# Kernel optimization log

Hardware: AMD Instinct MI355X
Metric: run time of the kernel (lower is better)

The kernel has to match this reference:

```python
import jax, jax.numpy as jnp
import numpy as np

T = 16          # time_span
N = 128         # num_trajectory
D = 512         # embedding dim
TEMP = 0.1      # temperature
INF = 1000000000.0
M = 2 * N * T   # total rows of z (two views)


def setup_inputs() -> dict:
    key = jax.random.key(0)
    k1, k2 = jax.random.split(key)
    z = jax.random.normal(k1, (M, D), dtype=jnp.float32)
    done = jax.random.randint(k2, (T, N), 0, 2).astype(jnp.int32)  # [T, N] binary done flags
    return {"z": z, "done": done}


def _build_positive_mask(done):
    # done: [T, N] int -> transposed to [N, T] as in the torch code
    d = done.astype(jnp.float32).T  # [N, T]
    # Sequential rewrite loop is equivalent to:
    #   done_new[r,t] = 1 iff exists original done at p < t in row r AND orig done[r,t] == 0
    excl = jnp.cumsum(d, axis=1) - d  # exclusive cumsum along time
    d_new = jnp.where((excl > 0) & (d == 0), 1.0, 0.0)  # [N, T]
    done_vec = 1.0 - d_new.reshape(-1)  # [N*T]
    # block-diagonal temporal mask: same trajectory => 1
    traj = jnp.arange(N * T) // T
    block = (traj[:, None] == traj[None, :]).astype(jnp.float32)  # [NT, NT]
    done_mask = (done_vec[:, None] * done_vec[None, :]) * block
    done_mask = jnp.tile(done_mask, (2, 2))      # [M, M]
    temporal_mask = jnp.tile(block, (2, 2))      # [M, M]
    eye = jnp.eye(M, dtype=jnp.float32)
    positive_mask = (1.0 - done_mask) * (1.0 - temporal_mask) + eye
    return positive_mask, eye


def reference(z, done):
    positive_mask, eye = _build_positive_mask(done)
    # cosine similarity = normalize + GEMM (same math as broadcasted F.cosine_similarity)
    norms = jnp.maximum(jnp.linalg.norm(z, axis=-1, keepdims=True), 1e-8)
    zn = z / norms
    logits = (zn @ zn.T) / TEMP - eye * INF  # [M, M]
    log_probs = jax.nn.log_softmax(logits, axis=1)
    neg = 1.0 - positive_mask
    mean_log_prob = jnp.sum(neg * log_probs, axis=1) / jnp.sum(neg, axis=1)
    return -jnp.mean(mean_log_prob)
```

## Files before the change

kernel.cpp:

```cpp
#include <hip/hip_runtime.h>
#include <hip/hip_bf16.h>

typedef float f32x16 __attribute__((ext_vector_type(16)));
typedef unsigned short u16;
typedef unsigned char u8;
typedef unsigned int u32;
typedef unsigned long long u64;


__device__ inline void async_cp16(const u8* g, u8* l) {
    __builtin_amdgcn_global_load_lds(
        (const __attribute__((address_space(1))) unsigned int*)g,
        (__attribute__((address_space(3))) unsigned int*)l, 16, 0, 0);
}

__global__ void nrm_kernel(const float* __restrict__ z, u8* __restrict__ zn8) {
    int row = blockIdx.x;
    int tid = threadIdx.x;
    float4 v = ((const float4*)(z + row * 512))[tid];
    float ss = v.x * v.x + v.y * v.y + v.z * v.z + v.w * v.w;
#pragma unroll
    for (int off = 32; off; off >>= 1) ss += __shfl_down(ss, off, 64);
    __shared__ float red[2];
    if ((tid & 63) == 0) red[tid >> 6] = ss;
    __syncthreads();
    float sc = 1.0f / fmaxf(sqrtf(red[0] + red[1]), 1e-8f);
    u32 w = __builtin_amdgcn_cvt_pk_fp8_f32(v.x * sc, v.y * sc, 0, false);
    w = __builtin_amdgcn_cvt_pk_fp8_f32(v.z * sc, v.w * sc, w, true);
    ((u32*)(zn8 + (size_t)row * 512))[tid] = w;
}

__global__ void pos_kernel(const u8* __restrict__ zn8, float* __restrict__ possum) {
    int g = blockIdx.x;
    int l = threadIdx.x;
    int u = l & 31, h = l >> 5;
    int grow = (u < 16) ? (g * 16 + u) : (2048 + g * 16 + (u - 16));
    const u64* src = (const u64*)(zn8 + (size_t)grow * 512);
    f32x16 acc = {};
#pragma unroll
    for (int kc = 0; kc < 32; ++kc) {
        u64 f = src[2 * kc + h];
        acc = __builtin_amdgcn_mfma_f32_32x32x16_fp8_fp8((long)f, (long)f, acc, 0, 0, 0);
    }
#pragma unroll
    for (int r = 0; r < 16; ++r) {
        int rrow = (r & 3) + 8 * (r >> 2) + 4 * h;
        float v = (rrow == u) ? 0.f : acc[r];
        v += __shfl_xor(v, 1, 64);
        v += __shfl_xor(v, 2, 64);
        v += __shfl_xor(v, 4, 64);
        v += __shfl_xor(v, 8, 64);
        v += __shfl_xor(v, 16, 64);
        if (u == 0) {
            int gr = (rrow < 16) ? (g * 16 + rrow) : (2048 + g * 16 + (rrow - 16));
            possum[gr] = v * 10.0f;
        }
    }
}

__global__ __launch_bounds__(256, 3) void gemm_kernel(const u8* __restrict__ zn8,
                                                      float* __restrict__ part) {
    __shared__ u8 Bt[2][32 * 512];
    __shared__ float colred[4][4][32];
    __shared__ float rowred[128];
    int wave = threadIdx.x >> 6;
    int l = threadIdx.x & 63;
    int m = l & 31, h = l >> 5;

    int t = blockIdx.x, i = 0;
    while (t >= 32 - i) { t -= 32 - i; ++i; }
    int j = i + t;
    int rowbase = i * 128 + wave * 32;
    bool diagwg = (i == j);

    long af[32];
    {
        const u8* arow = zn8 + (size_t)(rowbase + m) * 512 + h * 8;
#pragma unroll
        for (int kc = 0; kc < 32; ++kc) af[kc] = *(const long*)(arow + kc * 16);
    }

    float expacc[16];
#pragma unroll
    for (int r = 0; r < 16; ++r) expacc[r] = 0.f;

    auto stage = [&](int buf, int ct) {
        int colbase = j * 128 + ct * 32;
#pragma unroll
        for (int it = 0; it < 4; ++it) {
            int c = wave * 8 + 2 * it;
            int C = colbase + c + h;
            int srcoff = (m ^ (C & 7)) * 16;
            async_cp16(zn8 + (size_t)C * 512 + srcoff, &Bt[buf][c * 512]);
        }
    };

    stage(0, 0);
    int sB16 = (m & 7) * 16;
    for (int ct = 0; ct < 4; ++ct) {
        __syncthreads();
        if (ct < 3) stage((ct + 1) & 1, ct + 1);
        const u8* bcol = &Bt[ct & 1][m * 512 + h * 8];
        f32x16 acc = {};
#pragma unroll
        for (int kc = 0; kc < 32; ++kc) {
            u64 bf = *(const u64*)(bcol + ((kc * 16) ^ sB16));
            acc = __builtin_amdgcn_mfma_f32_32x32x16_fp8_fp8(af[kc], (long)bf, acc, 0, 0, 0);
        }
        bool diagtile = diagwg && (ct == wave);
        float cs = 0.f;
#pragma unroll
        for (int r = 0; r < 16; ++r) {
            int rrow = (r & 3) + 8 * (r >> 2) + 4 * h;
            float e = (diagtile && rrow == m) ? 0.f : __expf(acc[r] * 10.0f);
            expacc[r] += e;
            cs += e;
        }
        cs += __shfl_xor(cs, 32, 64);
        if (h == 0) colred[wave][ct][m] = cs;
    }

#pragma unroll
    for (int r = 0; r < 16; ++r) {
        float v = expacc[r];
        v += __shfl_xor(v, 1, 64);
        v += __shfl_xor(v, 2, 64);
        v += __shfl_xor(v, 4, 64);
        v += __shfl_xor(v, 8, 64);
        v += __shfl_xor(v, 16, 64);
        if (m == 0) {
            int rrow = (r & 3) + 8 * (r >> 2) + 4 * h;
            rowred[wave * 32 + rrow] = v;
        }
    }
    __syncthreads();
    if (threadIdx.x < 128) {
        int tid = threadIdx.x;
        part[(size_t)(i * 32 + j) * 128 + tid] = rowred[tid];
        if (!diagwg) {
            int tt = tid >> 5, c2 = tid & 31;
            float cv = colred[0][tt][c2] + colred[1][tt][c2] +
                       colred[2][tt][c2] + colred[3][tt][c2];
            part[(size_t)(j * 32 + i) * 128 + tid] = cv;
        }
    }
}

__global__ void fin_kernel(const float* __restrict__ part,
                           const float* __restrict__ possum, float* __restrict__ out) {
    int tid = threadIdx.x;
    float s = 0.f;
    for (int r = tid; r < 4096; r += 1024) {
        int b = r >> 7, rr = r & 127;
        float es = 0.f;
#pragma unroll
        for (int sl = 0; sl < 32; ++sl) es += part[(size_t)(b * 32 + sl) * 128 + rr];
        s += __logf(es) - possum[r] * (1.0f / 31.0f);
    }
#pragma unroll
    for (int off = 32; off; off >>= 1) s += __shfl_down(s, off, 64);
    __shared__ float red[16];
    if ((tid & 63) == 0) red[tid >> 6] = s;
    __syncthreads();
    if (tid == 0) {
        float tt = 0.f;
#pragma unroll
        for (int i2 = 0; i2 < 16; ++i2) tt += red[i2];
        out[0] = tt * (1.0f / 4096.0f);
    }
}

extern "C" void kernel_launch(void* const* d_in, const int* in_sizes, int n_in,
                              void* d_out, int out_size, void* d_ws, size_t ws_size,
                              hipStream_t stream) {
    const float* z = (const float*)d_in[0];
    u8* zn8 = (u8*)d_ws;
    float* part = (float*)((char*)d_ws + (2u << 20));
    float* possum = part + 32 * 32 * 128;
    float* out = (float*)d_out;

    nrm_kernel<<<4096, 128, 0, stream>>>(z, zn8);
    pos_kernel<<<128, 64, 0, stream>>>(zn8, possum);
    gemm_kernel<<<528, 256, 0, stream>>>(zn8, part);
    fin_kernel<<<1, 1024, 0, stream>>>(part, possum, out);
}
```

Measured before the change: 99.40 us.

## Fuse normalize, positive-sum, GEMM and finalize into one persistent kernel with grid barriers

Replaces the four separate launches with a single persistent kernel of 512 workgroups that synchronise through atomic-counter grid barriers. Normalisation, the positive-sum MFMA pass, the tiled exp GEMM and the final log reduction now run as phases of that one kernel, and the last reduction is spread across all workgroups. The MFMA inner loop is also split into two independent accumulators to shorten the dependency chain. This removes launch gaps and the single-block finalize, at the cost of a memset, spin-wait barriers that require every workgroup to be co-resident, and 16 leftover GEMM jobs handled by a second loop iteration.

```diff
diff --git a/kernel.cpp b/kernel.cpp
--- a/kernel.cpp
+++ b/kernel.cpp
@@ -2,10 +2,11 @@
 #include <hip/hip_bf16.h>
 
 typedef float f32x16 __attribute__((ext_vector_type(16)));
-typedef unsigned short u16;
 typedef unsigned char u8;
 typedef unsigned int u32;
 typedef unsigned long long u64;
+
+#define NWG 512
 
 
 __device__ inline void async_cp16(const u8* g, u8* l) {
@@ -14,159 +15,192 @@
         (__attribute__((address_space(3))) unsigned int*)l, 16, 0, 0);
 }
 
-__global__ void nrm_kernel(const float* __restrict__ z, u8* __restrict__ zn8) {
-    int row = blockIdx.x;
-    int tid = threadIdx.x;
-    float4 v = ((const float4*)(z + row * 512))[tid];
-    float ss = v.x * v.x + v.y * v.y + v.z * v.z + v.w * v.w;
-#pragma unroll
-    for (int off = 32; off; off >>= 1) ss += __shfl_down(ss, off, 64);
-    __shared__ float red[2];
-    if ((tid & 63) == 0) red[tid >> 6] = ss;
+__device__ inline void gridbar(u32* ctr, int ph) {
+    __threadfence();
     __syncthreads();
-    float sc = 1.0f / fmaxf(sqrtf(red[0] + red[1]), 1e-8f);
-    u32 w = __builtin_amdgcn_cvt_pk_fp8_f32(v.x * sc, v.y * sc, 0, false);
-    w = __builtin_amdgcn_cvt_pk_fp8_f32(v.z * sc, v.w * sc, w, true);
-    ((u32*)(zn8 + (size_t)row * 512))[tid] = w;
-}
-
-__global__ void pos_kernel(const u8* __restrict__ zn8, float* __restrict__ possum) {
-    int g = blockIdx.x;
-    int l = threadIdx.x;
-    int u = l & 31, h = l >> 5;
-    int grow = (u < 16) ? (g * 16 + u) : (2048 + g * 16 + (u - 16));
-    const u64* src = (const u64*)(zn8 + (size_t)grow * 512);
-    f32x16 acc = {};
-#pragma unroll
-    for (int kc = 0; kc < 32; ++kc) {
-        u64 f = src[2 * kc + h];
-        acc = __builtin_amdgcn_mfma_f32_32x32x16_fp8_fp8((long)f, (long)f, acc, 0, 0, 0);
-    }
-#pragma unroll
-    for (int r = 0; r < 16; ++r) {
-        int rrow = (r & 3) + 8 * (r >> 2) + 4 * h;
-        float v = (rrow == u) ? 0.f : acc[r];
-        v += __shfl_xor(v, 1, 64);
-        v += __shfl_xor(v, 2, 64);
-        v += __shfl_xor(v, 4, 64);
-        v += __shfl_xor(v, 8, 64);
-        v += __shfl_xor(v, 16, 64);
-        if (u == 0) {
-            int gr = (rrow < 16) ? (g * 16 + rrow) : (2048 + g * 16 + (rrow - 16));
-            possum[gr] = v * 10.0f;
-        }
-    }
-}
-
-__global__ __launch_bounds__(256, 3) void gemm_kernel(const u8* __restrict__ zn8,
-                                                      float* __restrict__ part) {
+    if (threadIdx.x == 0) {
+        __hip_atomic_fetch_add(&ctr[ph], 1u, __ATOMIC_ACQ_REL, __HIP_MEMORY_SCOPE_AGENT);
+        while (__hip_atomic_load(&ctr[ph], __ATOMIC_ACQUIRE, __HIP_MEMORY_SCOPE_AGENT) < NWG)
+            __builtin_amdgcn_s_sleep(2);
+    }
+    __syncthreads();
+    __threadfence();
+}
+
+__global__ __launch_bounds__(256, 2) void mega_kernel(
+        const float* __restrict__ z, u8* __restrict__ zn8, float* __restrict__ part,
+        float* __restrict__ possum, float* __restrict__ wgsum, u32* __restrict__ ctr,
+        float* __restrict__ out) {
     __shared__ u8 Bt[2][32 * 512];
     __shared__ float colred[4][4][32];
     __shared__ float rowred[128];
-    int wave = threadIdx.x >> 6;
-    int l = threadIdx.x & 63;
-    int m = l & 31, h = l >> 5;
-
-    int t = blockIdx.x, i = 0;
-    while (t >= 32 - i) { t -= 32 - i; ++i; }
-    int j = i + t;
-    int rowbase = i * 128 + wave * 32;
-    bool diagwg = (i == j);
-
-    long af[32];
+    __shared__ float fred[8];
+    __shared__ float red2[4];
+
+    const int wg = blockIdx.x, tid = threadIdx.x;
+    const int wave = tid >> 6, l = tid & 63;
+    const int m = l & 31, h = l >> 5;
+
     {
+        int rl = tid >> 5, c = tid & 31;
+        size_t R = (size_t)wg * 8 + rl;
+        const float4* zr = (const float4*)(z + R * 512);
+        float4 v[4];
+        float ss = 0.f;
+#pragma unroll
+        for (int k = 0; k < 4; ++k) {
+            v[k] = zr[c + 32 * k];
+            ss += v[k].x * v[k].x + v[k].y * v[k].y + v[k].z * v[k].z + v[k].w * v[k].w;
+        }
+#pragma unroll
+        for (int off = 16; off; off >>= 1) ss += __shfl_xor(ss, off, 64);
+        float sc = 1.0f / fmaxf(sqrtf(ss), 1e-8f);
+        u32* zw = (u32*)(zn8 + R * 512);
+#pragma unroll
+        for (int k = 0; k < 4; ++k) {
+            u32 w = __builtin_amdgcn_cvt_pk_fp8_f32(v[k].x * sc, v[k].y * sc, 0, false);
+            w = __builtin_amdgcn_cvt_pk_fp8_f32(v[k].z * sc, v[k].w * sc, w, true);
+            zw[c + 32 * k] = w;
+        }
+    }
+    gridbar(ctr, 0);
+
+    for (int job = wg; job < 528; job += NWG) {
+        int t = job, i = 0;
+        while (t >= 32 - i) { t -= 32 - i; ++i; }
+        int j = i + t;
+        int rowbase = i * 128 + wave * 32;
+        bool diagwg = (i == j);
+
+        __syncthreads();
+
+        long af[32];
         const u8* arow = zn8 + (size_t)(rowbase + m) * 512 + h * 8;
 #pragma unroll
         for (int kc = 0; kc < 32; ++kc) af[kc] = *(const long*)(arow + kc * 16);
-    }
-
-    float expacc[16];
-#pragma unroll
-    for (int r = 0; r < 16; ++r) expacc[r] = 0.f;
-
-    auto stage = [&](int buf, int ct) {
-        int colbase = j * 128 + ct * 32;
-#pragma unroll
-        for (int it = 0; it < 4; ++it) {
-            int c = wave * 8 + 2 * it;
-            int C = colbase + c + h;
-            int srcoff = (m ^ (C & 7)) * 16;
-            async_cp16(zn8 + (size_t)C * 512 + srcoff, &Bt[buf][c * 512]);
-        }
-    };
-
-    stage(0, 0);
-    int sB16 = (m & 7) * 16;
-    for (int ct = 0; ct < 4; ++ct) {
-        __syncthreads();
-        if (ct < 3) stage((ct + 1) & 1, ct + 1);
-        const u8* bcol = &Bt[ct & 1][m * 512 + h * 8];
+
+        float expacc[16];
+#pragma unroll
+        for (int r = 0; r < 16; ++r) expacc[r] = 0.f;
+
+        {
+            int colbase = j * 128;
+#pragma unroll
+            for (int it = 0; it < 4; ++it) {
+                int c = wave * 8 + 2 * it;
+                int C = colbase + c + h;
+                async_cp16(zn8 + (size_t)C * 512 + (m ^ (C & 7)) * 16, &Bt[0][c * 512]);
+            }
+        }
+        int sB16 = (m & 7) * 16;
+        for (int ct = 0; ct < 4; ++ct) {
+            __syncthreads();
+            if (ct < 3) {
+                int colbase = j * 128 + (ct + 1) * 32;
+                u8* dstb = &Bt[(ct + 1) & 1][0];
+#pragma unroll
+                for (int it = 0; it < 4; ++it) {
+                    int c = wave * 8 + 2 * it;
+                    int C = colbase + c + h;
+                    async_cp16(zn8 + (size_t)C * 512 + (m ^ (C & 7)) * 16, dstb + c * 512);
+                }
+            }
+            const u8* bcol = &Bt[ct & 1][m * 512 + h * 8];
+            f32x16 acc0 = {}, acc1 = {};
+#pragma unroll
+            for (int kc = 0; kc < 16; ++kc) {
+                u64 b0 = *(const u64*)(bcol + (((2 * kc) * 16) ^ sB16));
+                u64 b1 = *(const u64*)(bcol + (((2 * kc + 1) * 16) ^ sB16));
+                acc0 = __builtin_amdgcn_mfma_f32_32x32x16_fp8_fp8(af[2 * kc], (long)b0, acc0, 0, 0, 0);
+                acc1 = __builtin_amdgcn_mfma_f32_32x32x16_fp8_fp8(af[2 * kc + 1], (long)b1, acc1, 0, 0, 0);
+            }
+            bool diagtile = diagwg && (ct == wave);
+            float cs = 0.f;
+#pragma unroll
+            for (int r = 0; r < 16; ++r) {
+                int rrow = (r & 3) + 8 * (r >> 2) + 4 * h;
+                float e = (diagtile && rrow == m) ? 0.f : __expf((acc0[r] + acc1[r]) * 10.0f);
+                expacc[r] += e;
+                cs += e;
+            }
+            cs += __shfl_xor(cs, 32, 64);
+            if (h == 0) colred[wave][ct][m] = cs;
+        }
+#pragma unroll
+        for (int r = 0; r < 16; ++r) {
+            float v = expacc[r];
+            v += __shfl_xor(v, 1, 64);
+            v += __shfl_xor(v, 2, 64);
+            v += __shfl_xor(v, 4, 64);
+            v += __shfl_xor(v, 8, 64);
+            v += __shfl_xor(v, 16, 64);
+            if (m == 0) rowred[wave * 32 + ((r & 3) + 8 * (r >> 2) + 4 * h)] = v;
+        }
+        __syncthreads();
+        if (tid < 128) {
+            part[(size_t)(i * 32 + j) * 128 + tid] = rowred[tid];
+            if (!diagwg) {
+                int tt = tid >> 5, c2 = tid & 31;
+                part[(size_t)(j * 32 + i) * 128 + tid] =
+                    colred[0][tt][c2] + colred[1][tt][c2] +
+                    colred[2][tt][c2] + colred[3][tt][c2];
+            }
+        }
+    }
+    if (wg >= 384 && wg < 416) {
+        int g = (wg - 384) * 4 + wave;
+        int u = m;
+        int grow = (u < 16) ? (g * 16 + u) : (2048 + g * 16 + (u - 16));
+        const u64* src = (const u64*)(zn8 + (size_t)grow * 512);
         f32x16 acc = {};
 #pragma unroll
         for (int kc = 0; kc < 32; ++kc) {
-            u64 bf = *(const u64*)(bcol + ((kc * 16) ^ sB16));
-            acc = __builtin_amdgcn_mfma_f32_32x32x16_fp8_fp8(af[kc], (long)bf, acc, 0, 0, 0);
-        }
-        bool diagtile = diagwg && (ct == wave);
-        float cs = 0.f;
+            u64 f = src[2 * kc + h];
+            acc = __builtin_amdgcn_mfma_f32_32x32x16_fp8_fp8((long)f, (long)f, acc, 0, 0, 0);
+        }
 #pragma unroll
         for (int r = 0; r < 16; ++r) {
             int rrow = (r & 3) + 8 * (r >> 2) + 4 * h;
-            float e = (diagtile && rrow == m) ? 0.f : __expf(acc[r] * 10.0f);
-            expacc[r] += e;
-            cs += e;
-        }
-        cs += __shfl_xor(cs, 32, 64);
-        if (h == 0) colred[wave][ct][m] = cs;
-    }
-
-#pragma unroll
-    for (int r = 0; r < 16; ++r) {
-        float v = expacc[r];
-        v += __shfl_xor(v, 1, 64);
-        v += __shfl_xor(v, 2, 64);
-        v += __shfl_xor(v, 4, 64);
-        v += __shfl_xor(v, 8, 64);
-        v += __shfl_xor(v, 16, 64);
-        if (m == 0) {
-            int rrow = (r & 3) + 8 * (r >> 2) + 4 * h;
-            rowred[wave * 32 + rrow] = v;
-        }
-    }
-    __syncthreads();
-    if (threadIdx.x < 128) {
-        int tid = threadIdx.x;
-        part[(size_t)(i * 32 + j) * 128 + tid] = rowred[tid];
-        if (!diagwg) {
-            int tt = tid >> 5, c2 = tid & 31;
-            float cv = colred[0][tt][c2] + colred[1][tt][c2] +
-                       colred[2][tt][c2] + colred[3][tt][c2];
-            part[(size_t)(j * 32 + i) * 128 + tid] = cv;
-        }
-    }
-}
-
-__global__ void fin_kernel(const float* __restrict__ part,
-                           const float* __restrict__ possum, float* __restrict__ out) {
-    int tid = threadIdx.x;
-    float s = 0.f;
-    for (int r = tid; r < 4096; r += 1024) {
-        int b = r >> 7, rr = r & 127;
-        float es = 0.f;
-#pragma unroll
-        for (int sl = 0; sl < 32; ++sl) es += part[(size_t)(b * 32 + sl) * 128 + rr];
-        s += __logf(es) - possum[r] * (1.0f / 31.0f);
-    }
-#pragma unroll
-    for (int off = 32; off; off >>= 1) s += __shfl_down(s, off, 64);
-    __shared__ float red[16];
-    if ((tid & 63) == 0) red[tid >> 6] = s;
-    __syncthreads();
-    if (tid == 0) {
-        float tt = 0.f;
-#pragma unroll
-        for (int i2 = 0; i2 < 16; ++i2) tt += red[i2];
-        out[0] = tt * (1.0f / 4096.0f);
+            float v = (rrow == u) ? 0.f : acc[r];
+            v += __shfl_xor(v, 1, 64);
+            v += __shfl_xor(v, 2, 64);
+            v += __shfl_xor(v, 4, 64);
+            v += __shfl_xor(v, 8, 64);
+            v += __shfl_xor(v, 16, 64);
+            if (u == 0) {
+                int gr = (rrow < 16) ? (g * 16 + rrow) : (2048 + g * 16 + (rrow - 16));
+                possum[gr] = v * 10.0f;
+            }
+        }
+    }
+    gridbar(ctr, 1);
+
+    {
+        int rl = tid >> 5, c = tid & 31;
+        int R = wg * 8 + rl;
+        int b = R >> 7, rr = R & 127;
+        float es = part[(size_t)(b * 32 + c) * 128 + rr];
+#pragma unroll
+        for (int off = 16; off; off >>= 1) es += __shfl_xor(es, off, 64);
+        if (c == 0) fred[rl] = __logf(es) - possum[R] * (1.0f / 31.0f);
+        __syncthreads();
+        if (tid == 0) {
+            float s = 0.f;
+#pragma unroll
+            for (int k = 0; k < 8; ++k) s += fred[k];
+            wgsum[wg] = s;
+        }
+    }
+    gridbar(ctr, 2);
+
+    if (wg == 0) {
+        float s = wgsum[tid] + wgsum[tid + 256];
+#pragma unroll
+        for (int off = 32; off; off >>= 1) s += __shfl_down(s, off, 64);
+        if (l == 0) red2[wave] = s;
+        __syncthreads();
+        if (tid == 0)
+            out[0] = (red2[0] + red2[1] + red2[2] + red2[3]) * (1.0f / 4096.0f);
     }
 }
 
@@ -177,10 +211,10 @@
     u8* zn8 = (u8*)d_ws;
     float* part = (float*)((char*)d_ws + (2u << 20));
     float* possum = part + 32 * 32 * 128;
+    float* wgsum = possum + 4096;
+    u32* ctr = (u32*)(wgsum + NWG);
     float* out = (float*)d_out;
 
-    nrm_kernel<<<4096, 128, 0, stream>>>(z, zn8);
-    pos_kernel<<<128, 64, 0, stream>>>(zn8, possum);
-    gemm_kernel<<<528, 256, 0, stream>>>(zn8, part);
-    fin_kernel<<<1, 1024, 0, stream>>>(part, possum, out);
-}
+    hipMemsetAsync(ctr, 0, 64, stream);
+    mega_kernel<<<NWG, 256, 0, stream>>>(z, zn8, part, possum, wgsum, ctr, out);
+}
```

Measured after the change: 360.9 us. 3.63x slower.
